# Kernel tuning notes

Measured on AMD Instinct MI355X. Metric: run time of the kernel, lower is better.

## Reference

```python
import jax, jax.numpy as jnp
import numpy as np

N, CIN, H, W = 32, 1024, 32, 32
C, CT, L = 1024, 1024, 16
HEAD, GROUPS = 16, 16
GS = C // GROUPS  # 64, group size == head dim


def setup_inputs() -> dict:
    key = jax.random.key(0)
    ks = jax.random.split(key, 8)
    s = 0.02
    return {
        "feature": jax.random.normal(ks[0], (N, CIN, H, W), jnp.float32),
        "token": jax.random.normal(ks[1], (N, CT, L), jnp.float32),
        # conv_query: Conv1d(CT, C, k=1) -> dense [C, CT] + bias [C]
        "Wq": jax.random.normal(ks[2], (C, CT), jnp.float32) * s,
        "bq": jax.random.normal(ks[3], (C,), jnp.float32) * s,
        # conv_key / conv_value: grouped Conv2d(C, C, k=1, groups=16) -> block-diag [G, GS, GS]
        "Wk": jax.random.normal(ks[4], (GROUPS, GS, GS), jnp.float32) * s,
        "bk": jax.random.normal(ks[5], (C,), jnp.float32) * s,
        "Wv": jax.random.normal(ks[6], (GROUPS, GS, GS), jnp.float32) * s,
        "bv": jax.random.normal(ks[7], (C,), jnp.float32) * s,
    }


def reference(feature, token, Wq, bq, Wk, bk, Wv, bv):
    n, c, h, w = feature.shape  # c == C (feature-proj branch skipped)
    hw = h * w
    hd = C // HEAD  # 64
    l = token.shape[2]

    # conv_query (1x1 conv1d == dense over channels): [N, C, L]
    query = jnp.einsum('oc,ncl->nol', Wq, token) + bq[None, :, None]
    query = query.reshape(n, HEAD, hd, l)  # [N, head, hd, L]

    # grouped 1x1 convs == per-group 64x64 matmul over spatial positions
    f = feature.reshape(n, GROUPS, GS, hw)  # [N, G, GS, HW]
    key_ = jnp.einsum('goi,ngix->ngox', Wk, f) + bk.reshape(1, GROUPS, GS, 1)
    key_ = key_.reshape(n, HEAD, hd, hw)  # groups == head, same channel layout
    value = jnp.einsum('goi,ngix->ngox', Wv, f) + bv.reshape(1, GROUPS, GS, 1)
    value = value.reshape(n, HEAD, hd, hw)

    # cross attention: coef[n,h,x,l] = <key[:,x], query[:,l]> / sqrt(hd)
    coef = jnp.einsum('nhdx,nhdl->nhxl', key_, query) / jnp.sqrt(jnp.asarray(hd, jnp.float32))
    coef = jax.nn.softmax(coef, axis=2)  # softmax over spatial dim HW

    tok = jnp.einsum('nhdx,nhxl->nhdl', value, coef)  # [N, head, hd, L]
    # torch: .view(N, C, -1).view(N, L, C) — raw memory reshape, NOT transpose
    tok = tok.reshape(n, C, l).reshape(n, l, C)
    return (feature, tok)
```

## Files before the change

kernel.cpp:

```cpp
#include <hip/hip_runtime.h>
#include <math.h>

#define NB    32
#define NHEAD 16
#define HW    1024

typedef float f32x4  __attribute__((ext_vector_type(4)));
typedef short bf16x2 __attribute__((ext_vector_type(2)));
typedef short bf16x4 __attribute__((ext_vector_type(4)));
typedef short bf16x8 __attribute__((ext_vector_type(8)));

__device__ __forceinline__ short f2bf(float f) {
    union { float f; unsigned u; } c; c.f = f;
    unsigned r = c.u + 0x7FFFu + ((c.u >> 16) & 1u);
    return (short)(r >> 16);
}
#define SWZ(row) ((((row) >> 1) & 7) << 4)
#define MFMA16(a, b, c) __builtin_amdgcn_mfma_f32_16x16x32_bf16(a, b, c, 0, 0, 0)

__device__ __forceinline__ bf16x8 lds_ld8(const short* base, int off) {
    return *(const bf16x8*)((const char*)base + off);
}
__device__ __forceinline__ void lds_st4(short* base, int off, bf16x4 v) {
    *(bf16x4*)((char*)base + off) = v;
}

__global__ __launch_bounds__(256) void prep_kernel(
        const float* __restrict__ Wq, const float* __restrict__ token,
        const float* __restrict__ Wk, const float* __restrict__ bq,
        short* __restrict__ Wq_bf, short* __restrict__ tok_t,
        short* __restrict__ Wk_t, float* __restrict__ qkb) {
    __shared__ float red[256];
    const int b = blockIdx.x, t = threadIdx.x;
    if (b < 1024) {
        const size_t idx = (size_t)b * 1024 + t * 4;
        const f32x4 v = *(const f32x4*)(Wq + idx);
        bf16x4 o; o[0]=f2bf(v[0]); o[1]=f2bf(v[1]); o[2]=f2bf(v[2]); o[3]=f2bf(v[3]);
        *(bf16x4*)(Wq_bf + idx) = o;
    } else if (b < 1056) {
        const int n = b - 1024;
        const int c0 = t * 4;
        float arr[4][16];
#pragma unroll
        for (int ci = 0; ci < 4; ++ci)
#pragma unroll
            for (int lq = 0; lq < 4; ++lq) {
                const f32x4 v = *(const f32x4*)(token + (size_t)n*16384 + (size_t)(c0+ci)*16 + lq*4);
#pragma unroll
                for (int e = 0; e < 4; ++e) arr[ci][lq*4+e] = v[e];
            }
#pragma unroll
        for (int l = 0; l < 16; ++l) {
            bf16x4 o; o[0]=f2bf(arr[0][l]); o[1]=f2bf(arr[1][l]); o[2]=f2bf(arr[2][l]); o[3]=f2bf(arr[3][l]);
            *(bf16x4*)(tok_t + (size_t)n*16384 + (size_t)l*1024 + c0) = o;
        }
    } else {
        const int h = b - 1056;
        const int i = t & 63, dq = t >> 6;
        float qs = 0.f; short wt[16];
#pragma unroll
        for (int k = 0; k < 16; ++k) {
            const int d = dq*16 + k;
            const float wv = Wk[(size_t)h*4096 + d*64 + i];
            qs += wv * bq[h*64 + d];
            wt[k] = f2bf(wv);
        }
#pragma unroll
        for (int kq = 0; kq < 4; ++kq) {
            bf16x4 o; o[0]=wt[kq*4]; o[1]=wt[kq*4+1]; o[2]=wt[kq*4+2]; o[3]=wt[kq*4+3];
            *(bf16x4*)(Wk_t + (size_t)h*4096 + i*64 + dq*16 + kq*4) = o;
        }
        red[t] = qs;
        __syncthreads();
        if (t < 64)
            qkb[h*64 + t] = (red[t] + red[t+64] + red[t+128] + red[t+192]) * 0.125f;
    }
}

__global__ __launch_bounds__(256) void queryqk_kernel(
        const short* __restrict__ Wq_bf, const short* __restrict__ tok_t,
        const short* __restrict__ Wk_t, const float* __restrict__ qkb,
        short* __restrict__ qk_bf) {
    __shared__ short q_ld[16 * 64];
    const int t = threadIdx.x, w = t >> 6, L = t & 63;
    const int lr = L & 15, hg = L >> 4;
    const int nh = blockIdx.x, n = nh >> 4, h = nh & 15;

    f32x4 acc = {0.f, 0.f, 0.f, 0.f};
    const short* aA = Wq_bf + (size_t)(h*64 + w*16 + lr) * 1024 + hg*8;
    const short* aB = tok_t + (size_t)n*16384 + (size_t)lr*1024 + hg*8;
#pragma unroll 4
    for (int ks = 0; ks < 32; ++ks) {
        const bf16x8 a = *(const bf16x8*)(aA + ks*32);
        const bf16x8 bb = *(const bf16x8*)(aB + ks*32);
        acc = MFMA16(a, bb, acc);
    }
    {
        bf16x4 qv; qv[0]=f2bf(acc[0]); qv[1]=f2bf(acc[1]); qv[2]=f2bf(acc[2]); qv[3]=f2bf(acc[3]);
        lds_st4(q_ld, (lr*128 + w*32 + hg*8) ^ SWZ(lr), qv);
    }
    __syncthreads();
    f32x4 a2 = {0.f, 0.f, 0.f, 0.f};
#pragma unroll
    for (int ks = 0; ks < 2; ++ks) {
        const bf16x8 a = *(const bf16x8*)(Wk_t + (size_t)h*4096 + (w*16 + lr)*64 + ks*32 + hg*8);
        const bf16x8 bb = lds_ld8(q_ld, (lr*128 + ks*64 + hg*16) ^ SWZ(lr));
        a2 = MFMA16(a, bb, a2);
    }
    const int i0 = w*16 + hg*4;
    bf16x4 qk4;
#pragma unroll
    for (int r = 0; r < 4; ++r)
        qk4[r] = f2bf(a2[r] * 0.125f + qkb[h*64 + i0 + r]);
    *(bf16x4*)(qk_bf + (size_t)nh*1024 + lr*64 + i0) = qk4;
}

__global__ __launch_bounds__(1024, 4) void attn_kernel(
        const float* __restrict__ feat, const short* __restrict__ qk_bf,
        const float* __restrict__ Wv, const float* __restrict__ bv,
        float* __restrict__ out0, float* __restrict__ out1) {
    __shared__ short f_stage[32768];
    __shared__ short p_ld[16 * 1024];
    __shared__ f32x4 fcp_red[8][4][64];
    __shared__ short wv_ld[64 * 64];
    __shared__ short fcn_ld[16 * 64];
    __shared__ float red_m[256], red_z[256];

    const int t = threadIdx.x, w = t >> 6, L = t & 63;
    const int lr = L & 15, hg = L >> 4;
    const int nh = blockIdx.x, n = nh >> 4, h = nh & 15;
    const size_t fbase = (size_t)n*1048576 + (size_t)h*65536;

    const bf16x8 qb0 = *(const bf16x8*)(qk_bf + (size_t)nh*1024 + lr*64 + hg*8);
    const bf16x8 qb1 = *(const bf16x8*)(qk_bf + (size_t)nh*1024 + lr*64 + 32 + hg*8);

    f32x4 S[4];
#pragma unroll
    for (int tl = 0; tl < 4; ++tl) S[tl] = (f32x4){0.f, 0.f, 0.f, 0.f};

    for (int c = 0; c < 2; ++c) {
        {
            const size_t rbase = fbase + (size_t)(c*32 + w*2) * 1024;
#pragma unroll
            for (int xr = 0; xr < 4; ++xr) {
                const int x0 = xr*256 + L*4;
                const f32x4 v0 = *(const f32x4*)(feat + rbase + x0);
                const f32x4 v1 = *(const f32x4*)(feat + rbase + 1024 + x0);
                *(f32x4*)(out0 + rbase + x0) = v0;
                *(f32x4*)(out0 + rbase + 1024 + x0) = v1;
#pragma unroll
                for (int j = 0; j < 4; ++j) {
                    const int x = x0 + j;
                    bf16x2 pr; pr[0] = f2bf(v0[j]); pr[1] = f2bf(v1[j]);
                    const int off = ((x>>1)<<7) + ((((x&1)<<6) + w*4) ^ (((x>>2)&7)<<4));
                    *(bf16x2*)((char*)f_stage + off) = pr;
                }
            }
        }
        __syncthreads();
        {
            const bf16x8 qb = c ? qb1 : qb0;
#pragma unroll
            for (int tl = 0; tl < 4; ++tl) {
                const int x = w*64 + tl*16 + lr;
                const int off = ((x>>1)<<7) + ((((x&1)<<6) + (hg<<4)) ^ (((x>>2)&7)<<4));
                const bf16x8 a = *(const bf16x8*)((const char*)f_stage + off);
                S[tl] = MFMA16(a, qb, S[tl]);
            }
        }
        __syncthreads();
    }

    float m_l = -INFINITY;
#pragma unroll
    for (int tl = 0; tl < 4; ++tl)
#pragma unroll
        for (int r = 0; r < 4; ++r) m_l = fmaxf(m_l, S[tl][r]);
    m_l = fmaxf(m_l, __shfl_xor(m_l, 16));
    m_l = fmaxf(m_l, __shfl_xor(m_l, 32));
    if (L < 16) red_m[w*16 + L] = m_l;
    __syncthreads();
    float m_g = -INFINITY;
#pragma unroll
    for (int k = 0; k < 16; ++k) m_g = fmaxf(m_g, red_m[k*16 + lr]);
    float zl = 0.f;
#pragma unroll
    for (int tl = 0; tl < 4; ++tl)
#pragma unroll
        for (int r = 0; r < 4; ++r) {
            S[tl][r] = __expf(S[tl][r] - m_g);
            zl += S[tl][r];
        }
#pragma unroll
    for (int tl = 0; tl < 4; ++tl) {
        bf16x4 pv; pv[0]=f2bf(S[tl][0]); pv[1]=f2bf(S[tl][1]); pv[2]=f2bf(S[tl][2]); pv[3]=f2bf(S[tl][3]);
        const int x0 = w*64 + tl*16 + hg*4;
        *(bf16x4*)((char*)p_ld + lr*2048 + ((x0*2) ^ ((lr&7)<<4))) = pv;
    }
    zl += __shfl_xor(zl, 16);
    zl += __shfl_xor(zl, 32);
    if (L < 16) red_z[w*16 + L] = zl;
    __syncthreads();
    float Zg = 0.f;
#pragma unroll
    for (int k = 0; k < 16; ++k) Zg += red_z[k*16 + lr];
    const float rz = 1.f / Zg;

    const f32x4 wv4 = *(const f32x4*)(Wv + (size_t)h*4096 + (t>>4)*64 + (t&15)*4);

    const int tile3 = w & 1;
    const int kslice = w >> 1;
    for (int c = 0; c < 2; ++c) {
        {
            const size_t rbase = fbase + (size_t)(c*32 + w*2) * 1024;
            const int il0 = w*2, il1 = w*2 + 1;
#pragma unroll
            for (int xr = 0; xr < 4; ++xr) {
                const int x0 = xr*256 + L*4;
                const f32x4 v0 = *(const f32x4*)(feat + rbase + x0);
                const f32x4 v1 = *(const f32x4*)(feat + rbase + 1024 + x0);
                bf16x4 b0; b0[0]=f2bf(v0[0]); b0[1]=f2bf(v0[1]); b0[2]=f2bf(v0[2]); b0[3]=f2bf(v0[3]);
                bf16x4 b1; b1[0]=f2bf(v1[0]); b1[1]=f2bf(v1[1]); b1[2]=f2bf(v1[2]); b1[3]=f2bf(v1[3]);
                *(bf16x4*)((char*)f_stage + il0*2048 + ((x0*2) ^ ((il0&7)<<4))) = b0;
                *(bf16x4*)((char*)f_stage + il1*2048 + ((x0*2) ^ ((il1&7)<<4))) = b1;
            }
        }
        __syncthreads();
        {
            f32x4 acc = {0.f, 0.f, 0.f, 0.f};
            const int il_m = tile3*16 + lr;
#pragma unroll
            for (int s = 0; s < 4; ++s) {
                const int ks = kslice*4 + s;
                const bf16x8 a = *(const bf16x8*)((const char*)f_stage
                        + il_m*2048 + (((ks*64) + (hg<<4)) ^ ((il_m&7)<<4)));
                const bf16x8 b = *(const bf16x8*)((const char*)p_ld
                        + lr*2048 + (((ks*64) + (hg<<4)) ^ ((lr&7)<<4)));
                acc = MFMA16(a, b, acc);
            }
            fcp_red[kslice][2*c + tile3][L] = acc;
        }
        __syncthreads();
    }

    if (w < 4) {
        f32x4 sum = fcp_red[0][w][L];
#pragma unroll
        for (int ks = 1; ks < 8; ++ks) sum += fcp_red[ks][w][L];
        bf16x4 fb;
#pragma unroll
        for (int r = 0; r < 4; ++r) fb[r] = f2bf(sum[r] * rz);
        const int i0 = w*16 + hg*4;
        *(bf16x4*)((char*)fcn_ld + lr*128 + ((i0*2) ^ ((lr&7)<<4))) = fb;
    }
    {
        const int d = t >> 4, i4 = (t & 15) * 4;
        bf16x4 wb; wb[0]=f2bf(wv4[0]); wb[1]=f2bf(wv4[1]); wb[2]=f2bf(wv4[2]); wb[3]=f2bf(wv4[3]);
        *(bf16x4*)((char*)wv_ld + d*128 + ((i4*2) ^ ((d&7)<<4))) = wb;
    }
    __syncthreads();
    if (w < 4) {
        f32x4 acc = {0.f, 0.f, 0.f, 0.f};
        const int d_m = w*16 + lr;
#pragma unroll
        for (int ks = 0; ks < 2; ++ks) {
            const bf16x8 a = *(const bf16x8*)((const char*)wv_ld
                    + d_m*128 + (((ks*64) + (hg<<4)) ^ ((d_m&7)<<4)));
            const bf16x8 b = *(const bf16x8*)((const char*)fcn_ld
                    + lr*128 + (((ks*64) + (hg<<4)) ^ ((lr&7)<<4)));
            acc = MFMA16(a, b, acc);
        }
#pragma unroll
        for (int r = 0; r < 4; ++r) {
            const int d = w*16 + hg*4 + r;
            out1[((size_t)n*1024 + h*64 + d)*16 + lr] = acc[r] + bv[h*64 + d];
        }
    }
}

extern "C" void kernel_launch(void* const* d_in, const int* in_sizes, int n_in,
                              void* d_out, int out_size, void* d_ws, size_t ws_size,
                              hipStream_t stream) {
    const float* feature = (const float*)d_in[0];
    const float* token   = (const float*)d_in[1];
    const float* Wq      = (const float*)d_in[2];
    const float* bq      = (const float*)d_in[3];
    const float* Wk      = (const float*)d_in[4];
    const float* Wv      = (const float*)d_in[6];
    const float* bv      = (const float*)d_in[7];

    float* out0 = (float*)d_out;
    float* out1 = out0 + (size_t)NB * 1024 * HW;

    short* Wq_bf = (short*)d_ws;
    short* tok_t = Wq_bf + (size_t)1024 * 1024;
    short* Wk_t  = tok_t + (size_t)NB * 16 * 1024;
    short* qk_bf = Wk_t + (size_t)NHEAD * 64 * 64;
    float* qkb   = (float*)(qk_bf + (size_t)NB * NHEAD * 1024);

    prep_kernel   <<<dim3(1072), 256, 0, stream>>>(Wq, token, Wk, bq, Wq_bf, tok_t, Wk_t, qkb);
    queryqk_kernel<<<dim3(NB * NHEAD), 256, 0, stream>>>(Wq_bf, tok_t, Wk_t, qkb, qk_bf);
    attn_kernel   <<<dim3(NB * NHEAD), 1024, 0, stream>>>(feature, qk_bf, Wv, bv, out0, out1);
}
```

Measured before the change: 88.42 us.

## Keep softmax P fragments in registers and split reduction by wave over x

The P matrix is no longer kept in a dedicated LDS buffer. Each wave reads its own P fragments into registers and then computes partial feature·P products over its own x-slice for all channel tiles. Partials are reduced through reused f_stage space rather than a separate fcp_red buffer. This lowers LDS use so the launch bound can claim higher occupancy, at the cost of an extra sync and a 16-way reduction in place of an 8-way one.

```diff
diff --git a/kernel.cpp b/kernel.cpp
--- a/kernel.cpp
+++ b/kernel.cpp
@@ -115,15 +115,13 @@
     *(bf16x4*)(qk_bf + (size_t)nh*1024 + lr*64 + i0) = qk4;
 }
 
-__global__ __launch_bounds__(1024, 4) void attn_kernel(
+__global__ __launch_bounds__(1024, 8) void attn_kernel(
         const float* __restrict__ feat, const short* __restrict__ qk_bf,
         const float* __restrict__ Wv, const float* __restrict__ bv,
         float* __restrict__ out0, float* __restrict__ out1) {
-    __shared__ short f_stage[32768];
-    __shared__ short p_ld[16 * 1024];
-    __shared__ f32x4 fcp_red[8][4][64];
-    __shared__ short wv_ld[64 * 64];
-    __shared__ short fcn_ld[16 * 64];
+    __shared__ __align__(16) short f_stage[32 * 1024];
+    __shared__ __align__(16) short wv_ld[64 * 64];
+    __shared__ __align__(16) short fcn_ld[16 * 64];
     __shared__ float red_m[256], red_z[256];
 
     const int t = threadIdx.x, w = t >> 6, L = t & 63;
@@ -194,8 +192,7 @@
 #pragma unroll
     for (int tl = 0; tl < 4; ++tl) {
         bf16x4 pv; pv[0]=f2bf(S[tl][0]); pv[1]=f2bf(S[tl][1]); pv[2]=f2bf(S[tl][2]); pv[3]=f2bf(S[tl][3]);
-        const int x0 = w*64 + tl*16 + hg*4;
-        *(bf16x4*)((char*)p_ld + lr*2048 + ((x0*2) ^ ((lr&7)<<4))) = pv;
+        *(bf16x4*)((char*)f_stage + w*2048 + lr*128 + (((tl*32 + hg*8)) ^ ((lr&7)<<4))) = pv;
     }
     zl += __shfl_xor(zl, 16);
     zl += __shfl_xor(zl, 32);
@@ -205,11 +202,13 @@
 #pragma unroll
     for (int k = 0; k < 16; ++k) Zg += red_z[k*16 + lr];
     const float rz = 1.f / Zg;
-
-    const f32x4 wv4 = *(const f32x4*)(Wv + (size_t)h*4096 + (t>>4)*64 + (t&15)*4);
-
-    const int tile3 = w & 1;
-    const int kslice = w >> 1;
+    const bf16x8 pb0 = *(const bf16x8*)((const char*)f_stage + w*2048 + lr*128 + ((      hg*16) ^ ((lr&7)<<4)));
+    const bf16x8 pb1 = *(const bf16x8*)((const char*)f_stage + w*2048 + lr*128 + ((64 + hg*16) ^ ((lr&7)<<4)));
+    __syncthreads();
+
+    f32x4 acc_fc[4];
+#pragma unroll
+    for (int ct = 0; ct < 4; ++ct) acc_fc[ct] = (f32x4){0.f, 0.f, 0.f, 0.f};
     for (int c = 0; c < 2; ++c) {
         {
             const size_t rbase = fbase + (size_t)(c*32 + w*2) * 1024;
@@ -227,47 +226,46 @@
         }
         __syncthreads();
         {
-            f32x4 acc = {0.f, 0.f, 0.f, 0.f};
-            const int il_m = tile3*16 + lr;
-#pragma unroll
-            for (int s = 0; s < 4; ++s) {
-                const int ks = kslice*4 + s;
-                const bf16x8 a = *(const bf16x8*)((const char*)f_stage
-                        + il_m*2048 + (((ks*64) + (hg<<4)) ^ ((il_m&7)<<4)));
-                const bf16x8 b = *(const bf16x8*)((const char*)p_ld
-                        + lr*2048 + (((ks*64) + (hg<<4)) ^ ((lr&7)<<4)));
-                acc = MFMA16(a, b, acc);
-            }
-            fcp_red[kslice][2*c + tile3][L] = acc;
-        }
-        __syncthreads();
-    }
-
-    if (w < 4) {
-        f32x4 sum = fcp_red[0][w][L];
-#pragma unroll
-        for (int ks = 1; ks < 8; ++ks) sum += fcp_red[ks][w][L];
-        bf16x4 fb;
-#pragma unroll
-        for (int r = 0; r < 4; ++r) fb[r] = f2bf(sum[r] * rz);
-        const int i0 = w*16 + hg*4;
-        *(bf16x4*)((char*)fcn_ld + lr*128 + ((i0*2) ^ ((lr&7)<<4))) = fb;
-    }
+#pragma unroll
+            for (int tl2 = 0; tl2 < 2; ++tl2) {
+                const int il_m = tl2*16 + lr;
+                const int base = il_m*2048, swz = (il_m&7)<<4;
+                const int ct = c*2 + tl2;
+                acc_fc[ct] = MFMA16(lds_ld8(f_stage, base + ((w*128      + hg*16) ^ swz)), pb0, acc_fc[ct]);
+                acc_fc[ct] = MFMA16(lds_ld8(f_stage, base + ((w*128 + 64 + hg*16) ^ swz)), pb1, acc_fc[ct]);
+            }
+        }
+        __syncthreads();
+    }
+
+#pragma unroll
+    for (int ct = 0; ct < 4; ++ct)
+        *(f32x4*)((char*)f_stage + w*4096 + ct*1024 + L*16) = acc_fc[ct];
     {
         const int d = t >> 4, i4 = (t & 15) * 4;
+        const f32x4 wv4 = *(const f32x4*)(Wv + (size_t)h*4096 + d*64 + i4);
         bf16x4 wb; wb[0]=f2bf(wv4[0]); wb[1]=f2bf(wv4[1]); wb[2]=f2bf(wv4[2]); wb[3]=f2bf(wv4[3]);
         *(bf16x4*)((char*)wv_ld + d*128 + ((i4*2) ^ ((d&7)<<4))) = wb;
     }
     __syncthreads();
     if (w < 4) {
-        f32x4 acc = {0.f, 0.f, 0.f, 0.f};
+        f32x4 sum = (f32x4){0.f, 0.f, 0.f, 0.f};
+#pragma unroll
+        for (int wp = 0; wp < 16; ++wp)
+            sum += *(const f32x4*)((const char*)f_stage + wp*4096 + w*1024 + L*16);
+        bf16x4 fb;
+#pragma unroll
+        for (int r = 0; r < 4; ++r) fb[r] = f2bf(sum[r] * rz);
+        *(bf16x4*)((char*)fcn_ld + lr*128 + ((w*32 + hg*8) ^ ((lr&7)<<4))) = fb;
+    }
+    __syncthreads();
+    if (w < 4) {
+        f32x4 acc = (f32x4){0.f, 0.f, 0.f, 0.f};
         const int d_m = w*16 + lr;
 #pragma unroll
         for (int ks = 0; ks < 2; ++ks) {
-            const bf16x8 a = *(const bf16x8*)((const char*)wv_ld
-                    + d_m*128 + (((ks*64) + (hg<<4)) ^ ((d_m&7)<<4)));
-            const bf16x8 b = *(const bf16x8*)((const char*)fcn_ld
-                    + lr*128 + (((ks*64) + (hg<<4)) ^ ((lr&7)<<4)));
+            const bf16x8 a = lds_ld8(wv_ld, d_m*128 + ((ks*64 + hg*16) ^ ((d_m&7)<<4)));
+            const bf16x8 b = lds_ld8(fcn_ld, lr*128 + ((ks*64 + hg*16) ^ ((lr&7)<<4)));
             acc = MFMA16(a, b, acc);
         }
 #pragma unroll
```

New measurement: 103.1 us. 1.17x slower.
